# Performance work log

Hardware: AMD Instinct MI355X
Metric: run time of the kernel (lower is better)

The kernel has to match this reference:

```python
import jax, jax.numpy as jnp
import numpy as np

N = 50000
E = 800000
IN_CH = 128
HID = 128
HEADS = 8
OUT_CH = 40
NEG_SLOPE = 0.2
BN_EPS = 1e-5


def gat_conv(x, src, dst, W, a_src, a_dst, bias, heads, ch, concat):
    # x: [N, F_in]; W: [heads*ch, F_in]; a_src/a_dst: [heads, ch]; bias: [heads*ch] or [ch]
    n = x.shape[0]
    h = (x @ W.T).reshape(n, heads, ch)                      # [N, H, C]
    alpha_src = (h * a_src[None]).sum(-1)                    # [N, H]
    alpha_dst = (h * a_dst[None]).sum(-1)                    # [N, H]
    e = alpha_src[src] + alpha_dst[dst]                      # [E, H]
    e = jax.nn.leaky_relu(e, NEG_SLOPE)
    # segment softmax over incoming edges of each destination node
    emax = jax.ops.segment_max(e, dst, num_segments=n)       # [N, H]
    ee = jnp.exp(e - emax[dst])
    denom = jax.ops.segment_sum(ee, dst, num_segments=n)     # [N, H]
    alpha = ee / (denom[dst] + 1e-16)                        # [E, H]
    msg = h[src] * alpha[:, :, None]                         # [E, H, C]
    out = jax.ops.segment_sum(msg, dst, num_segments=n)      # [N, H, C]
    out = out.reshape(n, heads * ch) if concat else out.mean(axis=1)
    return out + bias


def batch_norm_eval(x, gamma, beta, mean, var):
    return (x - mean) * jax.lax.rsqrt(var + BN_EPS) * gamma + beta


def setup_inputs() -> dict:
    key = jax.random.key(0)
    ks = jax.random.split(key, 16)
    ch = HID // HEADS  # 16
    s = 1.0 / np.sqrt(IN_CH)
    inp = {
        "x": jax.random.normal(ks[0], (N, IN_CH), dtype=jnp.float32),
        "edge_index": jax.random.randint(ks[1], (2, E), 0, N, dtype=jnp.int64),
        # layer 0
        "W0": jax.random.normal(ks[2], (HEADS * ch, IN_CH), jnp.float32) * s,
        "a_src0": jax.random.normal(ks[3], (HEADS, ch), jnp.float32) * 0.1,
        "a_dst0": jax.random.normal(ks[4], (HEADS, ch), jnp.float32) * 0.1,
        "b0": jnp.zeros((HID,), jnp.float32),
        "bn_g0": jnp.ones((HID,), jnp.float32),
        "bn_b0": jnp.zeros((HID,), jnp.float32),
        "bn_m0": jnp.zeros((HID,), jnp.float32),
        "bn_v0": jnp.ones((HID,), jnp.float32),
        # layer 1
        "W1": jax.random.normal(ks[5], (HEADS * ch, HID), jnp.float32) * (1.0 / np.sqrt(HID)),
        "a_src1": jax.random.normal(ks[6], (HEADS, ch), jnp.float32) * 0.1,
        "a_dst1": jax.random.normal(ks[7], (HEADS, ch), jnp.float32) * 0.1,
        "b1": jnp.zeros((HID,), jnp.float32),
        "bn_g1": jnp.ones((HID,), jnp.float32),
        "bn_b1": jnp.zeros((HID,), jnp.float32),
        "bn_m1": jnp.zeros((HID,), jnp.float32),
        "bn_v1": jnp.ones((HID,), jnp.float32),
        # output layer (heads=1, concat=False)
        "W2": jax.random.normal(ks[8], (OUT_CH, HID), jnp.float32) * (1.0 / np.sqrt(HID)),
        "a_src2": jax.random.normal(ks[9], (1, OUT_CH), jnp.float32) * 0.1,
        "a_dst2": jax.random.normal(ks[10], (1, OUT_CH), jnp.float32) * 0.1,
        "b2": jnp.zeros((OUT_CH,), jnp.float32),
    }
    return inp


def reference(x, edge_index, W0, a_src0, a_dst0, b0, bn_g0, bn_b0, bn_m0, bn_v0,
              W1, a_src1, a_dst1, b1, bn_g1, bn_b1, bn_m1, bn_v1,
              W2, a_src2, a_dst2, b2):
    n = x.shape[0]
    # PyG GATConv adds self-loops by default
    loops = jnp.arange(n, dtype=edge_index.dtype)
    src = jnp.concatenate([edge_index[0], loops])
    dst = jnp.concatenate([edge_index[1], loops])
    ch = HID // HEADS

    h = gat_conv(x, src, dst, W0, a_src0, a_dst0, b0, HEADS, ch, True)
    h = batch_norm_eval(h, bn_g0, bn_b0, bn_m0, bn_v0)
    h = jax.nn.elu(h)
    # dropout: eval mode (identity)

    h = gat_conv(h, src, dst, W1, a_src1, a_dst1, b1, HEADS, ch, True)
    h = batch_norm_eval(h, bn_g1, bn_b1, bn_m1, bn_v1)
    h = jax.nn.elu(h)

    out = gat_conv(h, src, dst, W2, a_src2, a_dst2, b2, 1, OUT_CH, False)
    return out
```

## Files before the change

kernel.cpp:

```cpp
#include <hip/hip_runtime.h>
#include <hip/hip_fp16.h>
#include <math.h>

constexpr float NEG_SLOPE = 0.2f;
constexpr float BN_EPS_C = 1e-5f;

using half8 = __attribute__((ext_vector_type(8))) _Float16;
using f32x4 = __attribute__((ext_vector_type(4))) float;


__global__ void cvt_w_kernel(const float* __restrict__ W0, const float* __restrict__ W1,
                             const float* __restrict__ W2,
                             __half* __restrict__ W0h, __half* __restrict__ W1h,
                             __half* __restrict__ W2h) {
    int i = blockIdx.x * blockDim.x + threadIdx.x;
    if (i < 16384) {
        W0h[i] = __float2half(W0[i]);
        W1h[i] = __float2half(W1[i]);
    }
    if (i < 6144) W2h[i] = __float2half(i < 5120 ? W2[i] : 0.f);
}


__global__ __launch_bounds__(256)
void bucket_hist_kernel(const int* __restrict__ ei, int* __restrict__ bucket_count,
                        int E, int N) {
    __shared__ int h[256];
    int t = threadIdx.x;
    h[t] = 0;
    __syncthreads();
    int base = blockIdx.x * 4096;
    int ET = E + N;
#pragma unroll
    for (int q = 0; q < 16; ++q) {
        int i = base + q * 256 + t;
        if (i < ET) {
            int d = (i < E) ? ei[E + i] : (i - E);
            atomicAdd(&h[d >> 8], 1);
        }
    }
    __syncthreads();
    if (h[t] > 0) atomicAdd(&bucket_count[t], h[t]);
}

__global__ __launch_bounds__(256)
void bucket_scan_kernel(const int* __restrict__ bucket_count, int* __restrict__ bucket_ptr,
                        int* __restrict__ gcursor, int* __restrict__ row_ptr,
                        int N, int ET) {
    __shared__ int s[256];
    int t = threadIdx.x;
    int c = bucket_count[t];
    s[t] = c;
    __syncthreads();
    for (int off = 1; off < 256; off <<= 1) {
        int v = (t >= off) ? s[t - off] : 0;
        __syncthreads();
        s[t] += v;
        __syncthreads();
    }
    int excl = s[t] - c;
    bucket_ptr[t] = excl;
    gcursor[t] = excl;
    if (t == 255) {
        bucket_ptr[256] = s[255];
        row_ptr[N] = ET;
    }
}

__global__ __launch_bounds__(256)
void bucket_bin_kernel(const int* __restrict__ ei, int* __restrict__ gcursor,
                       int2* __restrict__ tmp, int E, int N) {
    __shared__ int2 bins[4096];
    __shared__ int lcount[256];
    __shared__ int lofs[256];
    __shared__ int lbase[256];
    __shared__ int lcur[256];
    int t = threadIdx.x;
    lcount[t] = 0;
    __syncthreads();
    int base = blockIdx.x * 4096;
    int ET = E + N;
    int2 pr[16];
#pragma unroll
    for (int q = 0; q < 16; ++q) {
        int i = base + q * 256 + t;
        pr[q] = make_int2(-1, -1);
        if (i < ET) {
            int s, d;
            if (i < E) { s = ei[i]; d = ei[E + i]; }
            else       { s = i - E; d = s; }
            pr[q] = make_int2(d, s);
            atomicAdd(&lcount[d >> 8], 1);
        }
    }
    __syncthreads();
    {
        int c = lcount[t];
        lofs[t] = c;
        __syncthreads();
        for (int off = 1; off < 256; off <<= 1) {
            int v = (t >= off) ? lofs[t - off] : 0;
            __syncthreads();
            lofs[t] += v;
            __syncthreads();
        }
        int excl = lofs[t] - c;
        __syncthreads();
        lofs[t] = excl;
        lcur[t] = excl;
        if (c > 0) lbase[t] = atomicAdd(&gcursor[t], c);
    }
    __syncthreads();
#pragma unroll
    for (int q = 0; q < 16; ++q) {
        if (pr[q].x >= 0) {
            int b = pr[q].x >> 8;
            int p = atomicAdd(&lcur[b], 1);
            bins[p] = pr[q];
        }
    }
    __syncthreads();
    int total = min(4096, ET - base);
    for (int p = t; p < total; p += 256) {
        int2 e = bins[p];
        int b = e.x >> 8;
        tmp[lbase[b] + (p - lofs[b])] = e;
    }
}

__global__ __launch_bounds__(256)
void fine_scatter_kernel(const int2* __restrict__ tmp, const int* __restrict__ bucket_ptr,
                         int* __restrict__ row_ptr, int* __restrict__ srcs, int N) {
    __shared__ int hist[256];
    __shared__ int scanb[256];
    __shared__ int cur[256];
    int b = blockIdx.x, t = threadIdx.x;
    int base = bucket_ptr[b];
    int cnt = bucket_ptr[b + 1] - base;
    int n0 = b << 8;
    hist[t] = 0;
    __syncthreads();
    for (int p = t; p < cnt; p += 256)
        atomicAdd(&hist[tmp[base + p].x - n0], 1);
    __syncthreads();
    int c = hist[t];
    scanb[t] = c;
    __syncthreads();
    for (int off = 1; off < 256; off <<= 1) {
        int v = (t >= off) ? scanb[t - off] : 0;
        __syncthreads();
        scanb[t] += v;
        __syncthreads();
    }
    int excl = scanb[t] - c;
    cur[t] = excl;
    if (n0 + t < N) row_ptr[n0 + t] = base + excl;
    __syncthreads();
    for (int p = t; p < cnt; p += 256) {
        int2 e = tmp[base + p];
        int pos = atomicAdd(&cur[e.x - n0], 1);
        srcs[base + pos] = e.y;
    }
}


template<bool AHALF>
__global__ __launch_bounds__(256)
void gemm128_mfma_kernel(const void* __restrict__ Xv, const __half* __restrict__ W16,
                         const float* __restrict__ a_src, const float* __restrict__ a_dst,
                         __half* __restrict__ hp, float* __restrict__ asrc,
                         float* __restrict__ adst, int N) {
    __shared__ _Float16 Bs[128][136];
    const int t = threadIdx.x;
    const int n0 = blockIdx.x * 64;

#pragma unroll
    for (int i = 0; i < 8; ++i) {
        int lin = t + i * 256;
        int n = lin >> 4;
        int m = lin & 15;
        *reinterpret_cast<uint4*>(&Bs[n][8 * m]) =
            *reinterpret_cast<const uint4*>(&W16[(size_t)n * 128 + 8 * m]);
    }
    __syncthreads();

    const int l  = t & 63;
    const int w  = t >> 6;
    const int lr = l & 15;
    const int lg = l >> 4;
    const int rowA = n0 + 16 * w + lr;
    const bool rokA = rowA < N;

    f32x4 acc[8];
#pragma unroll
    for (int tt = 0; tt < 8; ++tt) acc[tt] = (f32x4){0.f, 0.f, 0.f, 0.f};

#pragma unroll
    for (int ks = 0; ks < 4; ++ks) {
        half8 a;
        if (rokA) {
            if constexpr (AHALF) {
                const __half* X = (const __half*)Xv;
                a = *reinterpret_cast<const half8*>(&X[(size_t)rowA * 128 + 8 * lg + 32 * ks]);
            } else {
                const float* X = (const float*)Xv;
                const float* p = &X[(size_t)rowA * 128 + 8 * lg + 32 * ks];
                float4 v0 = *reinterpret_cast<const float4*>(p);
                float4 v1 = *reinterpret_cast<const float4*>(p + 4);
                a[0] = (_Float16)v0.x; a[1] = (_Float16)v0.y;
                a[2] = (_Float16)v0.z; a[3] = (_Float16)v0.w;
                a[4] = (_Float16)v1.x; a[5] = (_Float16)v1.y;
                a[6] = (_Float16)v1.z; a[7] = (_Float16)v1.w;
            }
        } else {
#pragma unroll
            for (int q = 0; q < 8; ++q) a[q] = (_Float16)0.f;
        }
#pragma unroll
        for (int tt = 0; tt < 8; ++tt) {
            half8 b = *reinterpret_cast<const half8*>(&Bs[16 * tt + lr][8 * lg + 32 * ks]);
            acc[tt] = __builtin_amdgcn_mfma_f32_16x16x32_f16(a, b, acc[tt], 0, 0, 0);
        }
    }

    float av[8], bv[8];
#pragma unroll
    for (int tt = 0; tt < 8; ++tt) {
        av[tt] = a_src[16 * tt + lr];
        bv[tt] = a_dst[16 * tt + lr];
    }
#pragma unroll
    for (int reg = 0; reg < 4; ++reg) {
        int gr = n0 + 16 * w + 4 * lg + reg;
        bool ok = gr < N;
        if (ok) {
#pragma unroll
            for (int tt = 0; tt < 8; ++tt)
                hp[(size_t)gr * 128 + 16 * tt + lr] = __float2half(acc[tt][reg]);
        }
#pragma unroll
        for (int tt = 0; tt < 8; ++tt) {
            float p = acc[tt][reg] * av[tt];
            float q = acc[tt][reg] * bv[tt];
#pragma unroll
            for (int off = 1; off < 16; off <<= 1) {
                p += __shfl_xor(p, off, 16);
                q += __shfl_xor(q, off, 16);
            }
            if (ok && lr == tt) {
                asrc[(size_t)gr * 8 + tt] = p;
                adst[(size_t)gr * 8 + tt] = q;
            }
        }
    }
}


__global__ __launch_bounds__(256)
void gemm40_mfma_kernel(const __half* __restrict__ X, const __half* __restrict__ W16,
                        const float* __restrict__ a_src, const float* __restrict__ a_dst,
                        __half* __restrict__ hp, float* __restrict__ asrc,
                        float* __restrict__ adst, int N) {
    __shared__ _Float16 Bs[48][136];
    const int t = threadIdx.x;
    const int n0 = blockIdx.x * 64;

#pragma unroll
    for (int i = 0; i < 3; ++i) {
        int lin = t + i * 256;
        if (lin < 768) {
            int n = lin >> 4;
            int m = lin & 15;
            *reinterpret_cast<uint4*>(&Bs[n][8 * m]) =
                *reinterpret_cast<const uint4*>(&W16[(size_t)n * 128 + 8 * m]);
        }
    }
    __syncthreads();

    const int l  = t & 63;
    const int w  = t >> 6;
    const int lr = l & 15;
    const int lg = l >> 4;
    const int rowA = n0 + 16 * w + lr;
    const bool rokA = rowA < N;

    f32x4 acc[3];
#pragma unroll
    for (int tt = 0; tt < 3; ++tt) acc[tt] = (f32x4){0.f, 0.f, 0.f, 0.f};

#pragma unroll
    for (int ks = 0; ks < 4; ++ks) {
        half8 a;
        if (rokA) {
            a = *reinterpret_cast<const half8*>(&X[(size_t)rowA * 128 + 8 * lg + 32 * ks]);
        } else {
#pragma unroll
            for (int q = 0; q < 8; ++q) a[q] = (_Float16)0.f;
        }
#pragma unroll
        for (int tt = 0; tt < 3; ++tt) {
            half8 b = *reinterpret_cast<const half8*>(&Bs[16 * tt + lr][8 * lg + 32 * ks]);
            acc[tt] = __builtin_amdgcn_mfma_f32_16x16x32_f16(a, b, acc[tt], 0, 0, 0);
        }
    }

    float av[3], bv[3];
#pragma unroll
    for (int tt = 0; tt < 3; ++tt) {
        int j = 16 * tt + lr;
        av[tt] = (j < 40) ? a_src[j] : 0.f;
        bv[tt] = (j < 40) ? a_dst[j] : 0.f;
    }
#pragma unroll
    for (int reg = 0; reg < 4; ++reg) {
        int gr = n0 + 16 * w + 4 * lg + reg;
        bool ok = gr < N;
        float p = 0.f, q = 0.f;
#pragma unroll
        for (int tt = 0; tt < 3; ++tt) {
            int j = 16 * tt + lr;
            if (ok && j < 40) hp[(size_t)gr * 40 + j] = __float2half(acc[tt][reg]);
            p += acc[tt][reg] * av[tt];
            q += acc[tt][reg] * bv[tt];
        }
#pragma unroll
        for (int off = 1; off < 16; off <<= 1) {
            p += __shfl_xor(p, off, 16);
            q += __shfl_xor(q, off, 16);
        }
        if (ok && lr == 0) {
            asrc[gr] = p;
            adst[gr] = q;
        }
    }
}


__global__ __launch_bounds__(256)
void message128_kernel(const uint4* __restrict__ hh4, const int* __restrict__ row_ptr,
                       const int* __restrict__ srcs,
                       const float* __restrict__ asrc, const float* __restrict__ adst,
                       const float* __restrict__ bias,
                       const float* __restrict__ bn_g, const float* __restrict__ bn_b,
                       const float* __restrict__ bn_m, const float* __restrict__ bn_v,
                       __half* __restrict__ out16, int N) {
    int node = blockIdx.x * 8 + (threadIdx.x >> 5);
    if (node >= N) return;
    int tc = threadIdx.x & 31;
    int half_id = tc >> 4;
    int cl = tc & 15;
    int hd = cl >> 1;
    int beg = row_ptr[node], end = row_ptr[node + 1];
    float ad = adst[(size_t)node * 8 + hd];
    float ssum = 0.f;
    float acc[8];
#pragma unroll
    for (int q = 0; q < 8; ++q) acc[q] = 0.f;

    int j = beg;
    for (; j + 4 <= end; j += 4) {
        int sA = srcs[j + half_id];
        int sB = srcs[j + 2 + half_id];
        uint4 uA = hh4[(size_t)sA * 16 + cl];
        uint4 uB = hh4[(size_t)sB * 16 + cl];
        float eA = asrc[(size_t)sA * 8 + hd] + ad;
        float eB = asrc[(size_t)sB * 8 + hd] + ad;
        eA = (eA > 0.f) ? eA : NEG_SLOPE * eA;
        eB = (eB > 0.f) ? eB : NEG_SLOPE * eB;
        float wA = __expf(eA);
        float wB = __expf(eB);
        ssum += wA + wB;
        float2 a0 = __half22float2(*reinterpret_cast<const __half2*>(&uA.x));
        float2 a1 = __half22float2(*reinterpret_cast<const __half2*>(&uA.y));
        float2 a2 = __half22float2(*reinterpret_cast<const __half2*>(&uA.z));
        float2 a3 = __half22float2(*reinterpret_cast<const __half2*>(&uA.w));
        float2 b0 = __half22float2(*reinterpret_cast<const __half2*>(&uB.x));
        float2 b1 = __half22float2(*reinterpret_cast<const __half2*>(&uB.y));
        float2 b2 = __half22float2(*reinterpret_cast<const __half2*>(&uB.z));
        float2 b3 = __half22float2(*reinterpret_cast<const __half2*>(&uB.w));
        acc[0] += wA * a0.x + wB * b0.x; acc[1] += wA * a0.y + wB * b0.y;
        acc[2] += wA * a1.x + wB * b1.x; acc[3] += wA * a1.y + wB * b1.y;
        acc[4] += wA * a2.x + wB * b2.x; acc[5] += wA * a2.y + wB * b2.y;
        acc[6] += wA * a3.x + wB * b3.x; acc[7] += wA * a3.y + wB * b3.y;
    }
    for (; j + 2 <= end; j += 2) {
        int s = srcs[j + half_id];
        uint4 u = hh4[(size_t)s * 16 + cl];
        float e = asrc[(size_t)s * 8 + hd] + ad;
        e = (e > 0.f) ? e : NEG_SLOPE * e;
        float wgt = __expf(e);
        ssum += wgt;
        float2 f0 = __half22float2(*reinterpret_cast<const __half2*>(&u.x));
        float2 f1 = __half22float2(*reinterpret_cast<const __half2*>(&u.y));
        float2 f2 = __half22float2(*reinterpret_cast<const __half2*>(&u.z));
        float2 f3 = __half22float2(*reinterpret_cast<const __half2*>(&u.w));
        acc[0] += wgt * f0.x; acc[1] += wgt * f0.y;
        acc[2] += wgt * f1.x; acc[3] += wgt * f1.y;
        acc[4] += wgt * f2.x; acc[5] += wgt * f2.y;
        acc[6] += wgt * f3.x; acc[7] += wgt * f3.y;
    }
    if (j < end && half_id == 0) {
        int s = srcs[j];
        uint4 u = hh4[(size_t)s * 16 + cl];
        float e = asrc[(size_t)s * 8 + hd] + ad;
        e = (e > 0.f) ? e : NEG_SLOPE * e;
        float wgt = __expf(e);
        ssum += wgt;
        float2 f0 = __half22float2(*reinterpret_cast<const __half2*>(&u.x));
        float2 f1 = __half22float2(*reinterpret_cast<const __half2*>(&u.y));
        float2 f2 = __half22float2(*reinterpret_cast<const __half2*>(&u.z));
        float2 f3 = __half22float2(*reinterpret_cast<const __half2*>(&u.w));
        acc[0] += wgt * f0.x; acc[1] += wgt * f0.y;
        acc[2] += wgt * f1.x; acc[3] += wgt * f1.y;
        acc[4] += wgt * f2.x; acc[5] += wgt * f2.y;
        acc[6] += wgt * f3.x; acc[7] += wgt * f3.y;
    }
    ssum += __shfl_xor(ssum, 16);
#pragma unroll
    for (int q = 0; q < 8; ++q) acc[q] += __shfl_xor(acc[q], 16);

    if (half_id == 0) {
        float inv = 1.0f / (ssum + 1e-16f);
        int c = cl * 8;
        float r[8];
#pragma unroll
        for (int pp = 0; pp < 2; ++pp) {
            int cc = c + 4 * pp;
            float4 bi = *reinterpret_cast<const float4*>(&bias[cc]);
            float4 g  = *reinterpret_cast<const float4*>(&bn_g[cc]);
            float4 bb = *reinterpret_cast<const float4*>(&bn_b[cc]);
            float4 mm = *reinterpret_cast<const float4*>(&bn_m[cc]);
            float4 vv = *reinterpret_cast<const float4*>(&bn_v[cc]);
            r[4 * pp + 0] = (acc[4 * pp + 0] * inv + bi.x - mm.x) * rsqrtf(vv.x + BN_EPS_C) * g.x + bb.x;
            r[4 * pp + 1] = (acc[4 * pp + 1] * inv + bi.y - mm.y) * rsqrtf(vv.y + BN_EPS_C) * g.y + bb.y;
            r[4 * pp + 2] = (acc[4 * pp + 2] * inv + bi.z - mm.z) * rsqrtf(vv.z + BN_EPS_C) * g.z + bb.z;
            r[4 * pp + 3] = (acc[4 * pp + 3] * inv + bi.w - mm.w) * rsqrtf(vv.w + BN_EPS_C) * g.w + bb.w;
        }
        half8 o;
#pragma unroll
        for (int q = 0; q < 8; ++q) {
            float rv = (r[q] > 0.f) ? r[q] : expm1f(r[q]);
            o[q] = (_Float16)rv;
        }
        *reinterpret_cast<half8*>(&out16[(size_t)node * 128 + c]) = o;
    }
}


__global__ __launch_bounds__(256)
void message40_kernel(const uint2* __restrict__ hh2, const int* __restrict__ row_ptr,
                      const int* __restrict__ srcs,
                      const float* __restrict__ asrc, const float* __restrict__ adst,
                      const float* __restrict__ b2, float* __restrict__ out, int N) {
    int node = blockIdx.x * 16 + (threadIdx.x >> 4);
    if (node >= N) return;
    int tc = threadIdx.x & 15;
    int beg = row_ptr[node], end = row_ptr[node + 1];
    float ad = adst[node];
    float ssum = 0.f;
    float4 acc = make_float4(0.f, 0.f, 0.f, 0.f);
    int j = beg;
    for (; j + 2 <= end; j += 2) {
        int s0 = srcs[j];
        int s1 = srcs[j + 1];
        uint2 u0 = make_uint2(0u, 0u), u1 = make_uint2(0u, 0u);
        if (tc < 10) {
            u0 = hh2[(size_t)s0 * 10 + tc];
            u1 = hh2[(size_t)s1 * 10 + tc];
        }
        float e0 = asrc[s0] + ad;
        float e1 = asrc[s1] + ad;
        e0 = (e0 > 0.f) ? e0 : NEG_SLOPE * e0;
        e1 = (e1 > 0.f) ? e1 : NEG_SLOPE * e1;
        float w0 = __expf(e0);
        float w1 = __expf(e1);
        ssum += w0 + w1;
        float2 a0 = __half22float2(*reinterpret_cast<const __half2*>(&u0.x));
        float2 b0 = __half22float2(*reinterpret_cast<const __half2*>(&u0.y));
        float2 a1 = __half22float2(*reinterpret_cast<const __half2*>(&u1.x));
        float2 b1 = __half22float2(*reinterpret_cast<const __half2*>(&u1.y));
        acc.x += w0 * a0.x + w1 * a1.x;
        acc.y += w0 * a0.y + w1 * a1.y;
        acc.z += w0 * b0.x + w1 * b1.x;
        acc.w += w0 * b0.y + w1 * b1.y;
    }
    if (j < end) {
        int s0 = srcs[j];
        uint2 u0 = make_uint2(0u, 0u);
        if (tc < 10) u0 = hh2[(size_t)s0 * 10 + tc];
        float e0 = asrc[s0] + ad;
        e0 = (e0 > 0.f) ? e0 : NEG_SLOPE * e0;
        float w0 = __expf(e0);
        ssum += w0;
        float2 a0 = __half22float2(*reinterpret_cast<const __half2*>(&u0.x));
        float2 b0 = __half22float2(*reinterpret_cast<const __half2*>(&u0.y));
        acc.x += w0 * a0.x;
        acc.y += w0 * a0.y;
        acc.z += w0 * b0.x;
        acc.w += w0 * b0.y;
    }
    if (tc < 10) {
        float inv = 1.0f / (ssum + 1e-16f);
        int c = tc * 4;
        float4 bi = *reinterpret_cast<const float4*>(&b2[c]);
        *reinterpret_cast<float4*>(&out[(size_t)node * 40 + c]) =
            make_float4(acc.x * inv + bi.x, acc.y * inv + bi.y,
                        acc.z * inv + bi.z, acc.w * inv + bi.w);
    }
}


static inline char* align256(char* p) {
    return (char*)(((uintptr_t)p + 255) & ~(uintptr_t)255);
}

extern "C" void kernel_launch(void* const* d_in, const int* in_sizes, int n_in,
                              void* d_out, int out_size, void* d_ws, size_t ws_size,
                              hipStream_t stream) {
    const float* x   = (const float*)d_in[0];
    const int*   ei  = (const int*)d_in[1];
    const float* W0  = (const float*)d_in[2];
    const float* as0 = (const float*)d_in[3];
    const float* ad0 = (const float*)d_in[4];
    const float* b0  = (const float*)d_in[5];
    const float* g0  = (const float*)d_in[6];
    const float* bb0 = (const float*)d_in[7];
    const float* m0  = (const float*)d_in[8];
    const float* v0  = (const float*)d_in[9];
    const float* W1  = (const float*)d_in[10];
    const float* as1 = (const float*)d_in[11];
    const float* ad1 = (const float*)d_in[12];
    const float* b1  = (const float*)d_in[13];
    const float* g1  = (const float*)d_in[14];
    const float* bb1 = (const float*)d_in[15];
    const float* m1  = (const float*)d_in[16];
    const float* v1  = (const float*)d_in[17];
    const float* W2  = (const float*)d_in[18];
    const float* as2 = (const float*)d_in[19];
    const float* ad2 = (const float*)d_in[20];
    const float* b2  = (const float*)d_in[21];

    const int N  = in_sizes[0] / 128;
    const int E  = in_sizes[1] / 2;
    const int ET = E + N;
    const int NBUK = (N + 255) >> 8;
    const int NEB  = (ET + 4095) / 4096;

    char* wsp = (char*)d_ws;
    int* bucket_count = (int*)wsp;  wsp = align256(wsp + 256 * 4);
    int* bucket_ptr   = (int*)wsp;  wsp = align256(wsp + 257 * 4);
    int* gcursor      = (int*)wsp;  wsp = align256(wsp + 256 * 4);
    int* row_ptr      = (int*)wsp;  wsp = align256(wsp + (size_t)(N + 1) * 4);
    int2* tmp         = (int2*)wsp; wsp = align256(wsp + (size_t)ET * 8);
    int* srcs         = (int*)wsp;  wsp = align256(wsp + (size_t)ET * 4);
    __half* hh        = (__half*)wsp; wsp = align256(wsp + (size_t)N * 128 * 2);
    __half* h2        = (__half*)wsp; wsp = align256(wsp + (size_t)N * 40 * 2);
    __half* feat      = (__half*)wsp; wsp = align256(wsp + (size_t)N * 128 * 2);
    float* asr        = (float*)wsp;  wsp = align256(wsp + (size_t)N * 8 * 4);
    float* adt        = (float*)wsp;  wsp = align256(wsp + (size_t)N * 8 * 4);
    __half* W0h       = (__half*)wsp; wsp = align256(wsp + 16384 * 2);
    __half* W1h       = (__half*)wsp; wsp = align256(wsp + 16384 * 2);
    __half* W2h       = (__half*)wsp; wsp = align256(wsp + 6144 * 2);

    cvt_w_kernel<<<64, 256, 0, stream>>>(W0, W1, W2, W0h, W1h, W2h);

    hipMemsetAsync(bucket_count, 0, 256 * 4, stream);
    bucket_hist_kernel<<<NEB, 256, 0, stream>>>(ei, bucket_count, E, N);
    bucket_scan_kernel<<<1, 256, 0, stream>>>(bucket_count, bucket_ptr, gcursor, row_ptr, N, ET);
    bucket_bin_kernel<<<NEB, 256, 0, stream>>>(ei, gcursor, tmp, E, N);
    fine_scatter_kernel<<<NBUK, 256, 0, stream>>>(tmp, bucket_ptr, row_ptr, srcs, N);

    const int g64 = (N + 63) / 64;

    gemm128_mfma_kernel<false><<<g64, 256, 0, stream>>>(x, W0h, as0, ad0, hh, asr, adt, N);
    message128_kernel<<<(N + 7) / 8, 256, 0, stream>>>((const uint4*)hh, row_ptr, srcs, asr, adt,
                                                       b0, g0, bb0, m0, v0, feat, N);
    gemm128_mfma_kernel<true><<<g64, 256, 0, stream>>>(feat, W1h, as1, ad1, hh, asr, adt, N);
    message128_kernel<<<(N + 7) / 8, 256, 0, stream>>>((const uint4*)hh, row_ptr, srcs, asr, adt,
                                                       b1, g1, bb1, m1, v1, feat, N);
    gemm40_mfma_kernel<<<g64, 256, 0, stream>>>(feat, W2h, as2, ad2, h2, asr, adt, N);
    message40_kernel<<<(N + 15) / 16, 256, 0, stream>>>((const uint2*)h2, row_ptr, srcs,
                                                        asr, adt, b2, (float*)d_out, N);
}
```

Measured before the change: 209.7 us.

## Pack edge pairs into 32-bit words, fuse weight conversion, enlarge binning tiles

Fuses the fp32-to-fp16 weight conversion into the histogram kernel as extra blocks, which removes one launch. Edge (dst, src) pairs are packed into a single 32-bit word, halving the temporary buffer traffic during binning and scattering. Each binning block now handles 8192 edges instead of 4096. The message kernels load half8/half4 vectors and use fmaf loops. The packing assumes node ids fit in 16 bits; with N=50000 that holds, but the bucket index derived as the top byte of the packed word relies on the same limit.

```diff
diff --git a/kernel.cpp b/kernel.cpp
--- a/kernel.cpp
+++ b/kernel.cpp
@@ -6,33 +6,34 @@
 constexpr float BN_EPS_C = 1e-5f;
 
 using half8 = __attribute__((ext_vector_type(8))) _Float16;
+using half4 = __attribute__((ext_vector_type(4))) _Float16;
 using f32x4 = __attribute__((ext_vector_type(4))) float;
 
 
-__global__ void cvt_w_kernel(const float* __restrict__ W0, const float* __restrict__ W1,
-                             const float* __restrict__ W2,
-                             __half* __restrict__ W0h, __half* __restrict__ W1h,
-                             __half* __restrict__ W2h) {
-    int i = blockIdx.x * blockDim.x + threadIdx.x;
-    if (i < 16384) {
-        W0h[i] = __float2half(W0[i]);
-        W1h[i] = __float2half(W1[i]);
-    }
-    if (i < 6144) W2h[i] = __float2half(i < 5120 ? W2[i] : 0.f);
-}
-
-
-__global__ __launch_bounds__(256)
-void bucket_hist_kernel(const int* __restrict__ ei, int* __restrict__ bucket_count,
-                        int E, int N) {
+__global__ __launch_bounds__(256)
+void hist_cvt_kernel(const int* __restrict__ ei, int* __restrict__ bucket_count,
+                     int E, int N, int NEB,
+                     const float* __restrict__ W0, const float* __restrict__ W1,
+                     const float* __restrict__ W2,
+                     __half* __restrict__ W0h, __half* __restrict__ W1h,
+                     __half* __restrict__ W2h) {
+    int t = threadIdx.x;
+    if ((int)blockIdx.x >= NEB) {
+        int i = ((int)blockIdx.x - NEB) * 256 + t;
+        if (i < 16384) {
+            W0h[i] = __float2half(W0[i]);
+            W1h[i] = __float2half(W1[i]);
+        }
+        if (i < 6144) W2h[i] = __float2half(i < 5120 ? W2[i] : 0.f);
+        return;
+    }
     __shared__ int h[256];
-    int t = threadIdx.x;
     h[t] = 0;
     __syncthreads();
-    int base = blockIdx.x * 4096;
+    int base = blockIdx.x * 8192;
     int ET = E + N;
 #pragma unroll
-    for (int q = 0; q < 16; ++q) {
+    for (int q = 0; q < 32; ++q) {
         int i = base + q * 256 + t;
         if (i < ET) {
             int d = (i < E) ? ei[E + i] : (i - E);
@@ -69,8 +70,8 @@
 
 __global__ __launch_bounds__(256)
 void bucket_bin_kernel(const int* __restrict__ ei, int* __restrict__ gcursor,
-                       int2* __restrict__ tmp, int E, int N) {
-    __shared__ int2 bins[4096];
+                       unsigned* __restrict__ tmp, int E, int N) {
+    __shared__ unsigned bins[8192];
     __shared__ int lcount[256];
     __shared__ int lofs[256];
     __shared__ int lbase[256];
@@ -78,18 +79,18 @@
     int t = threadIdx.x;
     lcount[t] = 0;
     __syncthreads();
-    int base = blockIdx.x * 4096;
+    int base = blockIdx.x * 8192;
     int ET = E + N;
-    int2 pr[16];
-#pragma unroll
-    for (int q = 0; q < 16; ++q) {
+    unsigned pr[32];
+#pragma unroll
+    for (int q = 0; q < 32; ++q) {
         int i = base + q * 256 + t;
-        pr[q] = make_int2(-1, -1);
+        pr[q] = 0xFFFFFFFFu;
         if (i < ET) {
             int s, d;
             if (i < E) { s = ei[i]; d = ei[E + i]; }
             else       { s = i - E; d = s; }
-            pr[q] = make_int2(d, s);
+            pr[q] = ((unsigned)d << 16) | (unsigned)s;
             atomicAdd(&lcount[d >> 8], 1);
         }
     }
@@ -112,24 +113,24 @@
     }
     __syncthreads();
 #pragma unroll
-    for (int q = 0; q < 16; ++q) {
-        if (pr[q].x >= 0) {
-            int b = pr[q].x >> 8;
+    for (int q = 0; q < 32; ++q) {
+        if (pr[q] != 0xFFFFFFFFu) {
+            int b = pr[q] >> 24;
             int p = atomicAdd(&lcur[b], 1);
             bins[p] = pr[q];
         }
     }
     __syncthreads();
-    int total = min(4096, ET - base);
+    int total = min(8192, ET - base);
     for (int p = t; p < total; p += 256) {
-        int2 e = bins[p];
-        int b = e.x >> 8;
+        unsigned e = bins[p];
+        int b = e >> 24;
         tmp[lbase[b] + (p - lofs[b])] = e;
     }
 }
 
 __global__ __launch_bounds__(256)
-void fine_scatter_kernel(const int2* __restrict__ tmp, const int* __restrict__ bucket_ptr,
+void fine_scatter_kernel(const unsigned* __restrict__ tmp, const int* __restrict__ bucket_ptr,
                          int* __restrict__ row_ptr, int* __restrict__ srcs, int N) {
     __shared__ int hist[256];
     __shared__ int scanb[256];
@@ -141,7 +142,7 @@
     hist[t] = 0;
     __syncthreads();
     for (int p = t; p < cnt; p += 256)
-        atomicAdd(&hist[tmp[base + p].x - n0], 1);
+        atomicAdd(&hist[(int)(tmp[base + p] >> 16) - n0], 1);
     __syncthreads();
     int c = hist[t];
     scanb[t] = c;
@@ -157,9 +158,9 @@
     if (n0 + t < N) row_ptr[n0 + t] = base + excl;
     __syncthreads();
     for (int p = t; p < cnt; p += 256) {
-        int2 e = tmp[base + p];
-        int pos = atomicAdd(&cur[e.x - n0], 1);
-        srcs[base + pos] = e.y;
+        unsigned e = tmp[base + p];
+        int pos = atomicAdd(&cur[(int)(e >> 16) - n0], 1);
+        srcs[base + pos] = (int)(e & 0xFFFFu);
     }
 }
 
@@ -337,7 +338,7 @@
 
 
 __global__ __launch_bounds__(256)
-void message128_kernel(const uint4* __restrict__ hh4, const int* __restrict__ row_ptr,
+void message128_kernel(const __half* __restrict__ hh, const int* __restrict__ row_ptr,
                        const int* __restrict__ srcs,
                        const float* __restrict__ asrc, const float* __restrict__ adst,
                        const float* __restrict__ bias,
@@ -361,8 +362,8 @@
     for (; j + 4 <= end; j += 4) {
         int sA = srcs[j + half_id];
         int sB = srcs[j + 2 + half_id];
-        uint4 uA = hh4[(size_t)sA * 16 + cl];
-        uint4 uB = hh4[(size_t)sB * 16 + cl];
+        half8 vA = *reinterpret_cast<const half8*>(&hh[(size_t)sA * 128 + 8 * cl]);
+        half8 vB = *reinterpret_cast<const half8*>(&hh[(size_t)sB * 128 + 8 * cl]);
         float eA = asrc[(size_t)sA * 8 + hd] + ad;
         float eB = asrc[(size_t)sB * 8 + hd] + ad;
         eA = (eA > 0.f) ? eA : NEG_SLOPE * eA;
@@ -370,50 +371,31 @@
         float wA = __expf(eA);
         float wB = __expf(eB);
         ssum += wA + wB;
-        float2 a0 = __half22float2(*reinterpret_cast<const __half2*>(&uA.x));
-        float2 a1 = __half22float2(*reinterpret_cast<const __half2*>(&uA.y));
-        float2 a2 = __half22float2(*reinterpret_cast<const __half2*>(&uA.z));
-        float2 a3 = __half22float2(*reinterpret_cast<const __half2*>(&uA.w));
-        float2 b0 = __half22float2(*reinterpret_cast<const __half2*>(&uB.x));
-        float2 b1 = __half22float2(*reinterpret_cast<const __half2*>(&uB.y));
-        float2 b2 = __half22float2(*reinterpret_cast<const __half2*>(&uB.z));
-        float2 b3 = __half22float2(*reinterpret_cast<const __half2*>(&uB.w));
-        acc[0] += wA * a0.x + wB * b0.x; acc[1] += wA * a0.y + wB * b0.y;
-        acc[2] += wA * a1.x + wB * b1.x; acc[3] += wA * a1.y + wB * b1.y;
-        acc[4] += wA * a2.x + wB * b2.x; acc[5] += wA * a2.y + wB * b2.y;
-        acc[6] += wA * a3.x + wB * b3.x; acc[7] += wA * a3.y + wB * b3.y;
+#pragma unroll
+        for (int q = 0; q < 8; ++q) {
+            acc[q] = fmaf((float)vA[q], wA, acc[q]);
+            acc[q] = fmaf((float)vB[q], wB, acc[q]);
+        }
     }
     for (; j + 2 <= end; j += 2) {
         int s = srcs[j + half_id];
-        uint4 u = hh4[(size_t)s * 16 + cl];
+        half8 v = *reinterpret_cast<const half8*>(&hh[(size_t)s * 128 + 8 * cl]);
         float e = asrc[(size_t)s * 8 + hd] + ad;
         e = (e > 0.f) ? e : NEG_SLOPE * e;
         float wgt = __expf(e);
         ssum += wgt;
-        float2 f0 = __half22float2(*reinterpret_cast<const __half2*>(&u.x));
-        float2 f1 = __half22float2(*reinterpret_cast<const __half2*>(&u.y));
-        float2 f2 = __half22float2(*reinterpret_cast<const __half2*>(&u.z));
-        float2 f3 = __half22float2(*reinterpret_cast<const __half2*>(&u.w));
-        acc[0] += wgt * f0.x; acc[1] += wgt * f0.y;
-        acc[2] += wgt * f1.x; acc[3] += wgt * f1.y;
-        acc[4] += wgt * f2.x; acc[5] += wgt * f2.y;
-        acc[6] += wgt * f3.x; acc[7] += wgt * f3.y;
+#pragma unroll
+        for (int q = 0; q < 8; ++q) acc[q] = fmaf((float)v[q], wgt, acc[q]);
     }
     if (j < end && half_id == 0) {
         int s = srcs[j];
-        uint4 u = hh4[(size_t)s * 16 + cl];
+        half8 v = *reinterpret_cast<const half8*>(&hh[(size_t)s * 128 + 8 * cl]);
         float e = asrc[(size_t)s * 8 + hd] + ad;
         e = (e > 0.f) ? e : NEG_SLOPE * e;
         float wgt = __expf(e);
         ssum += wgt;
-        float2 f0 = __half22float2(*reinterpret_cast<const __half2*>(&u.x));
-        float2 f1 = __half22float2(*reinterpret_cast<const __half2*>(&u.y));
-        float2 f2 = __half22float2(*reinterpret_cast<const __half2*>(&u.z));
-        float2 f3 = __half22float2(*reinterpret_cast<const __half2*>(&u.w));
-        acc[0] += wgt * f0.x; acc[1] += wgt * f0.y;
-        acc[2] += wgt * f1.x; acc[3] += wgt * f1.y;
-        acc[4] += wgt * f2.x; acc[5] += wgt * f2.y;
-        acc[6] += wgt * f3.x; acc[7] += wgt * f3.y;
+#pragma unroll
+        for (int q = 0; q < 8; ++q) acc[q] = fmaf((float)v[q], wgt, acc[q]);
     }
     ssum += __shfl_xor(ssum, 16);
 #pragma unroll
@@ -448,7 +430,7 @@
 
 
 __global__ __launch_bounds__(256)
-void message40_kernel(const uint2* __restrict__ hh2, const int* __restrict__ row_ptr,
+void message40_kernel(const __half* __restrict__ hh2, const int* __restrict__ row_ptr,
                       const int* __restrict__ srcs,
                       const float* __restrict__ asrc, const float* __restrict__ adst,
                       const float* __restrict__ b2, float* __restrict__ out, int N) {
@@ -458,15 +440,15 @@
     int beg = row_ptr[node], end = row_ptr[node + 1];
     float ad = adst[node];
     float ssum = 0.f;
-    float4 acc = make_float4(0.f, 0.f, 0.f, 0.f);
+    float acc[4] = {0.f, 0.f, 0.f, 0.f};
     int j = beg;
     for (; j + 2 <= end; j += 2) {
         int s0 = srcs[j];
         int s1 = srcs[j + 1];
-        uint2 u0 = make_uint2(0u, 0u), u1 = make_uint2(0u, 0u);
+        half4 v0 = (half4){0, 0, 0, 0}, v1 = (half4){0, 0, 0, 0};
         if (tc < 10) {
-            u0 = hh2[(size_t)s0 * 10 + tc];
-            u1 = hh2[(size_t)s1 * 10 + tc];
+            v0 = *reinterpret_cast<const half4*>(&hh2[(size_t)s0 * 40 + 4 * tc]);
+            v1 = *reinterpret_cast<const half4*>(&hh2[(size_t)s1 * 40 + 4 * tc]);
         }
         float e0 = asrc[s0] + ad;
         float e1 = asrc[s1] + ad;
@@ -475,37 +457,30 @@
         float w0 = __expf(e0);
         float w1 = __expf(e1);
         ssum += w0 + w1;
-        float2 a0 = __half22float2(*reinterpret_cast<const __half2*>(&u0.x));
-        float2 b0 = __half22float2(*reinterpret_cast<const __half2*>(&u0.y));
-        float2 a1 = __half22float2(*reinterpret_cast<const __half2*>(&u1.x));
-        float2 b1 = __half22float2(*reinterpret_cast<const __half2*>(&u1.y));
-        acc.x += w0 * a0.x + w1 * a1.x;
-        acc.y += w0 * a0.y + w1 * a1.y;
-        acc.z += w0 * b0.x + w1 * b1.x;
-        acc.w += w0 * b0.y + w1 * b1.y;
+#pragma unroll
+        for (int q = 0; q < 4; ++q) {
+            acc[q] = fmaf((float)v0[q], w0, acc[q]);
+            acc[q] = fmaf((float)v1[q], w1, acc[q]);
+        }
     }
     if (j < end) {
         int s0 = srcs[j];
-        uint2 u0 = make_uint2(0u, 0u);
-        if (tc < 10) u0 = hh2[(size_t)s0 * 10 + tc];
+        half4 v0 = (half4){0, 0, 0, 0};
+        if (tc < 10) v0 = *reinterpret_cast<const half4*>(&hh2[(size_t)s0 * 40 + 4 * tc]);
         float e0 = asrc[s0] + ad;
         e0 = (e0 > 0.f) ? e0 : NEG_SLOPE * e0;
         float w0 = __expf(e0);
         ssum += w0;
-        float2 a0 = __half22float2(*reinterpret_cast<const __half2*>(&u0.x));
-        float2 b0 = __half22float2(*reinterpret_cast<const __half2*>(&u0.y));
-        acc.x += w0 * a0.x;
-        acc.y += w0 * a0.y;
-        acc.z += w0 * b0.x;
-        acc.w += w0 * b0.y;
+#pragma unroll
+        for (int q = 0; q < 4; ++q) acc[q] = fmaf((float)v0[q], w0, acc[q]);
     }
     if (tc < 10) {
         float inv = 1.0f / (ssum + 1e-16f);
         int c = tc * 4;
         float4 bi = *reinterpret_cast<const float4*>(&b2[c]);
         *reinterpret_cast<float4*>(&out[(size_t)node * 40 + c]) =
-            make_float4(acc.x * inv + bi.x, acc.y * inv + bi.y,
-                        acc.z * inv + bi.z, acc.w * inv + bi.w);
+            make_float4(acc[0] * inv + bi.x, acc[1] * inv + bi.y,
+                        acc[2] * inv + bi.z, acc[3] * inv + bi.w);
     }
 }
 
@@ -544,14 +519,14 @@
     const int E  = in_sizes[1] / 2;
     const int ET = E + N;
     const int NBUK = (N + 255) >> 8;
-    const int NEB  = (ET + 4095) / 4096;
+    const int NEB  = (ET + 8191) / 8192;
 
     char* wsp = (char*)d_ws;
     int* bucket_count = (int*)wsp;  wsp = align256(wsp + 256 * 4);
     int* bucket_ptr   = (int*)wsp;  wsp = align256(wsp + 257 * 4);
     int* gcursor      = (int*)wsp;  wsp = align256(wsp + 256 * 4);
     int* row_ptr      = (int*)wsp;  wsp = align256(wsp + (size_t)(N + 1) * 4);
-    int2* tmp         = (int2*)wsp; wsp = align256(wsp + (size_t)ET * 8);
+    unsigned* tmp     = (unsigned*)wsp; wsp = align256(wsp + (size_t)ET * 4);
     int* srcs         = (int*)wsp;  wsp = align256(wsp + (size_t)ET * 4);
     __half* hh        = (__half*)wsp; wsp = align256(wsp + (size_t)N * 128 * 2);
     __half* h2        = (__half*)wsp; wsp = align256(wsp + (size_t)N * 40 * 2);
@@ -562,10 +537,9 @@
     __half* W1h       = (__half*)wsp; wsp = align256(wsp + 16384 * 2);
     __half* W2h       = (__half*)wsp; wsp = align256(wsp + 6144 * 2);
 
-    cvt_w_kernel<<<64, 256, 0, stream>>>(W0, W1, W2, W0h, W1h, W2h);
-
     hipMemsetAsync(bucket_count, 0, 256 * 4, stream);
-    bucket_hist_kernel<<<NEB, 256, 0, stream>>>(ei, bucket_count, E, N);
+    hist_cvt_kernel<<<NEB + 64, 256, 0, stream>>>(ei, bucket_count, E, N, NEB,
+                                                  W0, W1, W2, W0h, W1h, W2h);
     bucket_scan_kernel<<<1, 256, 0, stream>>>(bucket_count, bucket_ptr, gcursor, row_ptr, N, ET);
     bucket_bin_kernel<<<NEB, 256, 0, stream>>>(ei, gcursor, tmp, E, N);
     fine_scatter_kernel<<<NBUK, 256, 0, stream>>>(tmp, bucket_ptr, row_ptr, srcs, N);
@@ -573,12 +547,12 @@
     const int g64 = (N + 63) / 64;
 
     gemm128_mfma_kernel<false><<<g64, 256, 0, stream>>>(x, W0h, as0, ad0, hh, asr, adt, N);
-    message128_kernel<<<(N + 7) / 8, 256, 0, stream>>>((const uint4*)hh, row_ptr, srcs, asr, adt,
+    message128_kernel<<<(N + 7) / 8, 256, 0, stream>>>(hh, row_ptr, srcs, asr, adt,
                                                        b0, g0, bb0, m0, v0, feat, N);
     gemm128_mfma_kernel<true><<<g64, 256, 0, stream>>>(feat, W1h, as1, ad1, hh, asr, adt, N);
-    message128_kernel<<<(N + 7) / 8, 256, 0, stream>>>((const uint4*)hh, row_ptr, srcs, asr, adt,
+    message128_kernel<<<(N + 7) / 8, 256, 0, stream>>>(hh, row_ptr, srcs, asr, adt,
                                                        b1, g1, bb1, m1, v1, feat, N);
     gemm40_mfma_kernel<<<g64, 256, 0, stream>>>(feat, W2h, as2, ad2, h2, asr, adt, N);
-    message40_kernel<<<(N + 15) / 16, 256, 0, stream>>>((const uint2*)h2, row_ptr, srcs,
+    message40_kernel<<<(N + 15) / 16, 256, 0, stream>>>(h2, row_ptr, srcs,
                                                         asr, adt, b2, (float*)d_out, N);
 }
```

Result: no change. 213.8 us (+1.9%).
